# Kernel optimization log

Hardware: AMD Instinct MI355X
Metric: run time of the kernel (lower is better)

The kernel has to match this reference:

```python
import jax, jax.numpy as jnp
import numpy as np

NUM_ITER = 3
HEADS = 8
EPS = 1e-8

def _ln(x, g, b, eps=1e-5):
    mu = x.mean(-1, keepdims=True)
    var = ((x - mu) ** 2).mean(-1, keepdims=True)
    return (x - mu) * jax.lax.rsqrt(var + eps) * g + b

def setup_inputs() -> dict:
    key = jax.random.key(0)
    ks = jax.random.split(key, 10)
    B, Nkv, Din = 32, 4096, 256
    Nq, S, Hm = 16, 256, 512
    def xav(k, shape):
        lim = (6.0 / (shape[0] + shape[1])) ** 0.5
        return jax.random.uniform(k, shape, minval=-lim, maxval=lim, dtype=jnp.float32)
    return {
        "slots": jax.random.normal(ks[0], (Nq, S), dtype=jnp.float32),
        "inputs": jax.random.normal(ks[1], (B, Nkv, Din), dtype=jnp.float32),
        "norm_in_g": jnp.ones((Din,), jnp.float32), "norm_in_b": jnp.zeros((Din,), jnp.float32),
        "norm_slots_g": jnp.ones((S,), jnp.float32), "norm_slots_b": jnp.zeros((S,), jnp.float32),
        "norm_mlp_g": jnp.ones((S,), jnp.float32), "norm_mlp_b": jnp.zeros((S,), jnp.float32),
        "Wq": xav(ks[2], (S, S)), "Wk": xav(ks[3], (S, Din)), "Wv": xav(ks[4], (S, Din)),
        "gru_wih": xav(ks[5], (3 * S, S)),
        "gru_whh": jax.random.normal(ks[6], (3 * S, S), dtype=jnp.float32) * (1.0 / S ** 0.5),
        "gru_bih": jnp.zeros((3 * S,), jnp.float32), "gru_bhh": jnp.zeros((3 * S,), jnp.float32),
        "mlp_w1": xav(ks[7], (Hm, S)), "mlp_b1": jnp.zeros((Hm,), jnp.float32),
        "mlp_w2": xav(ks[8], (S, Hm)), "mlp_b2": jnp.zeros((S,), jnp.float32),
    }

def reference(slots, inputs, norm_in_g, norm_in_b, norm_slots_g, norm_slots_b,
              norm_mlp_g, norm_mlp_b, Wq, Wk, Wv, gru_wih, gru_whh, gru_bih, gru_bhh,
              mlp_w1, mlp_b1, mlp_w2, mlp_b2):
    B, Nkv, Din = inputs.shape
    Nq, S = slots.shape
    H = HEADS
    hd = S // H
    slots = jnp.broadcast_to(slots, (B, Nq, S))
    x = _ln(inputs, norm_in_g, norm_in_b)
    k = (x @ Wk.T).reshape(B, Nkv, H, hd).transpose(0, 2, 1, 3) * (hd ** -0.5)  # [B,H,Nkv,hd]
    v = (x @ Wv.T).reshape(B, Nkv, H, hd).transpose(0, 2, 1, 3)
    attn_vis = None
    for _ in range(NUM_ITER):
        slots_prev = slots
        s = _ln(slots, norm_slots_g, norm_slots_b)
        q = (s @ Wq.T).reshape(B, Nq, H, hd).transpose(0, 2, 1, 3)  # [B,H,Nq,hd]
        # logits [B,Nkv,H*Nq]; softmax jointly over heads and slots per key (slot-axis softmax)
        logits = jnp.einsum('bhkd,bhqd->bkhq', k, q).reshape(B, Nkv, H * Nq)
        attn = jax.nn.softmax(logits, axis=-1).reshape(B, Nkv, H, Nq).transpose(0, 2, 1, 3)  # [B,H,Nkv,Nq]
        attn_vis = attn.sum(1)  # [B,Nkv,Nq]
        attn_n = attn / (attn.sum(axis=2, keepdims=True) + EPS)  # normalize over keys
        updates = jnp.einsum('bhkq,bhkd->bqhd', attn_n, v).reshape(B, Nq, S)
        # GRUCell: gates order r,z,n
        xg = updates.reshape(-1, S)
        h = slots_prev.reshape(-1, S)
        gi = xg @ gru_wih.T + gru_bih
        gh = h @ gru_whh.T + gru_bhh
        ir, iz, inn = jnp.split(gi, 3, axis=-1)
        hr, hz, hn = jnp.split(gh, 3, axis=-1)
        r = jax.nn.sigmoid(ir + hr)
        z = jax.nn.sigmoid(iz + hz)
        n = jnp.tanh(inn + r * hn)
        slots = ((1.0 - z) * n + z * h).reshape(B, Nq, S)
        m = _ln(slots, norm_mlp_g, norm_mlp_b)
        slots = slots + (jax.nn.relu(m @ mlp_w1.T + mlp_b1) @ mlp_w2.T + mlp_b2)
    return (slots, attn_vis)
```

## Files before the change

kernel.cpp:

```cpp
#include <hip/hip_runtime.h>
#include <stdint.h>

typedef unsigned short u16;
typedef __attribute__((ext_vector_type(8))) _Float16 half8;
typedef __attribute__((ext_vector_type(4))) _Float16 half4;
typedef __attribute__((ext_vector_type(4))) float floatx4;

__device__ inline float bflo(unsigned u){ return __uint_as_float(u << 16); }
__device__ inline float bfhi(unsigned u){ return __uint_as_float(u & 0xffff0000u); }
__device__ inline float bf1(u16 v){ return __uint_as_float(((unsigned)v) << 16); }
__device__ inline u16 f2bf(float f){
  unsigned u = __float_as_uint(f);
  u += 0x7fffu + ((u >> 16) & 1u);
  return (u16)(u >> 16);
}
__device__ inline float dot8(uint4 w, float4 a, float4 b, float acc){
  acc = fmaf(bflo(w.x), a.x, acc); acc = fmaf(bfhi(w.x), a.y, acc);
  acc = fmaf(bflo(w.y), a.z, acc); acc = fmaf(bfhi(w.y), a.w, acc);
  acc = fmaf(bflo(w.z), b.x, acc); acc = fmaf(bfhi(w.z), b.y, acc);
  acc = fmaf(bflo(w.w), b.z, acc); acc = fmaf(bfhi(w.w), b.w, acc);
  return acc;
}

#define CW_SLOTS 0
#define CW_GIN   4096
#define CW_BIN   4352
#define CW_GS    4608
#define CW_BS    4864
#define CW_GM    5120
#define CW_BM    5376
#define CW_WQ    5632
#define CW_WK    71168
#define CW_WV    136704
#define CW_WIH   202240
#define CW_WHH   398848
#define CW_BIH   595456
#define CW_BHH   596224
#define CW_W1    596992
#define CW_B1    728064
#define CW_W2    728576
#define CW_B2    859648
#define CW_TOTAL 859904

__global__ void k_flag(const u16* __restrict__ probe, int* __restrict__ flag){
  int t = threadIdx.x;
  int bad = 0;
  #pragma unroll
  for (int i = 0; i < 4; i++){
    float x = bf1(probe[t + i * 256]);
    if (!(fabsf(x) < 1e6f)) bad = 1;
  }
  __shared__ int s;
  if (t == 0) s = 0;
  __syncthreads();
  if (bad) atomicOr(&s, 1);
  __syncthreads();
  if (t == 0) *flag = s;
}

struct CanonArgs { const void* p[18]; };

__global__ void k_canon(CanonArgs a, const int* __restrict__ flag, u16* __restrict__ cw){
  const int off[19] = {CW_SLOTS, CW_GIN, CW_BIN, CW_GS, CW_BS, CW_GM, CW_BM, CW_WQ,
                       CW_WK, CW_WV, CW_WIH, CW_WHH, CW_BIH, CW_BHH, CW_W1, CW_B1,
                       CW_W2, CW_B2, CW_TOTAL};
  int i = blockIdx.x * 256 + threadIdx.x;
  if (i >= CW_TOTAL) return;
  int f32m = *flag;
  int j = 0;
  while (i >= off[j + 1]) j++;
  int local = i - off[j];
  float v = f32m ? ((const float*)a.p[j])[local] : bf1(((const u16*)a.p[j])[local]);
  cw[i] = f2bf(v);
}

__global__ void k_init(const u16* __restrict__ cw, float* __restrict__ slots,
                       _Float16* __restrict__ wkvh)
{
  int idx = blockIdx.x * 256 + threadIdx.x;
  if (idx < 131072){
    float g = bf1(cw[CW_GIN + (idx & 255)]);
    wkvh[idx] = (_Float16)(bf1(cw[CW_WK + idx]) * g);
  } else {
    int i = idx - 131072;
    int d = i & 255;
    int q = (i >> 8) & 15;
    slots[i] = bf1(cw[CW_SLOTS + q * 256 + d]);
  }
}

__global__ void k_beta(const u16* __restrict__ cw, float* __restrict__ beta){
  int c = blockIdx.x * 256 + threadIdx.x;
  if (c >= 512) return;
  float a = 0.f;
  for (int d = 0; d < 256; d++)
    a = fmaf(bf1(cw[CW_BIN + d]), bf1(cw[CW_WK + c * 256 + d]), a);
  beta[c] = a;
}

__global__ void k_zero(float* __restrict__ p, int n){
  int i = blockIdx.x * 256 + threadIdx.x;
  if (i < n) p[i] = 0.f;
}

__global__ __launch_bounds__(256) void k0_stats(
    const void* __restrict__ inp, const int* __restrict__ flag, float2* __restrict__ stats)
{
  int f32m = *flag;
  int g = blockIdx.x * 256 + threadIdx.x;
  int row = g >> 4, l = g & 15;
  float sum = 0.f, sq = 0.f;
  if (f32m){
    const float* rp = (const float*)inp + row * 256 + l * 16;
    #pragma unroll
    for (int i = 0; i < 4; i++){
      float4 v = ((const float4*)rp)[i];
      sum += v.x + v.y + v.z + v.w;
      sq = fmaf(v.x, v.x, sq); sq = fmaf(v.y, v.y, sq);
      sq = fmaf(v.z, v.z, sq); sq = fmaf(v.w, v.w, sq);
    }
  } else {
    const u16* rp = (const u16*)inp + row * 256 + l * 16;
    #pragma unroll
    for (int i = 0; i < 2; i++){
      uint4 u = ((const uint4*)rp)[i];
      unsigned w[4] = {u.x, u.y, u.z, u.w};
      #pragma unroll
      for (int p = 0; p < 4; p++){
        float a = bflo(w[p]), b = bfhi(w[p]);
        sum += a + b; sq = fmaf(a, a, sq); sq = fmaf(b, b, sq);
      }
    }
  }
  #pragma unroll
  for (int m = 1; m < 16; m <<= 1){ sum += __shfl_xor(sum, m); sq += __shfl_xor(sq, m); }
  if (l == 0){
    float mu = sum * (1.f/256.f);
    float var = sq * (1.f/256.f) - mu * mu;
    stats[row] = make_float2(mu, rsqrtf(var + 1e-5f));
  }
}

__global__ __launch_bounds__(256) void k1_gemm(
    const void* __restrict__ inp, const int* __restrict__ flag,
    const float2* __restrict__ stats, const float* __restrict__ beta,
    const _Float16* __restrict__ wkvh, _Float16* __restrict__ kh, _Float16* __restrict__ vT)
{
  int f32m = *flag;
  int tid = threadIdx.x;
  int wv = tid >> 6, lane = tid & 63;
  int m16 = lane & 15, q4 = lane >> 4;
  int nb = blockIdx.y;
  long rowb0 = (long)blockIdx.x * 256;
  int colW = nb * 256 + wv * 64;

  half8 bf[4][8];
  #pragma unroll
  for (int nt = 0; nt < 4; nt++)
    #pragma unroll
    for (int s = 0; s < 8; s++)
      bf[nt][s] = *(const half8*)(wkvh + (colW + nt * 16 + m16) * 256 + s * 32 + q4 * 8);

  float bet[4];
  #pragma unroll
  for (int nt = 0; nt < 4; nt++) bet[nt] = beta[colW + nt * 16 + m16];

  for (int rt = 0; rt < 16; rt++){
    long rowb = rowb0 + rt * 16;
    long myRow = rowb + m16;
    float2 st = stats[myRow];
    float mu = st.x, rstd = st.y;

    half8 af[8];
    if (f32m){
      const float* rp = (const float*)inp + myRow * 256 + q4 * 8;
      #pragma unroll
      for (int s = 0; s < 8; s++){
        float4 x0 = *(const float4*)(rp + s * 32);
        float4 x1 = *(const float4*)(rp + s * 32 + 4);
        af[s][0] = (_Float16)((x0.x - mu) * rstd); af[s][1] = (_Float16)((x0.y - mu) * rstd);
        af[s][2] = (_Float16)((x0.z - mu) * rstd); af[s][3] = (_Float16)((x0.w - mu) * rstd);
        af[s][4] = (_Float16)((x1.x - mu) * rstd); af[s][5] = (_Float16)((x1.y - mu) * rstd);
        af[s][6] = (_Float16)((x1.z - mu) * rstd); af[s][7] = (_Float16)((x1.w - mu) * rstd);
      }
    } else {
      const u16* rp = (const u16*)inp + myRow * 256 + q4 * 8;
      #pragma unroll
      for (int s = 0; s < 8; s++){
        uint4 xu = *(const uint4*)(rp + s * 32);
        unsigned xw[4] = {xu.x, xu.y, xu.z, xu.w};
        #pragma unroll
        for (int p = 0; p < 4; p++){
          af[s][2*p]   = (_Float16)((bflo(xw[p]) - mu) * rstd);
          af[s][2*p+1] = (_Float16)((bfhi(xw[p]) - mu) * rstd);
        }
      }
    }

    floatx4 acc[4];
    #pragma unroll
    for (int nt = 0; nt < 4; nt++){
      acc[nt][0] = bet[nt]; acc[nt][1] = bet[nt]; acc[nt][2] = bet[nt]; acc[nt][3] = bet[nt];
    }
    #pragma unroll
    for (int s = 0; s < 8; s++)
      #pragma unroll
      for (int nt = 0; nt < 4; nt++)
        acc[nt] = __builtin_amdgcn_mfma_f32_16x16x32_f16(af[s], bf[nt][s], acc[nt], 0, 0, 0);

    if (nb == 0){
      long crow = rowb + q4 * 4;
      #pragma unroll
      for (int nt = 0; nt < 4; nt++)
        #pragma unroll
        for (int r = 0; r < 4; r++)
          kh[(crow + r) * 256 + colW + nt * 16 + m16] = (_Float16)acc[nt][r];
    } else {
      int b = (int)(rowb >> 12);
      int key = ((int)rowb & 4095) + q4 * 4;
      #pragma unroll
      for (int nt = 0; nt < 4; nt++){
        int cv = (colW - 256) + nt * 16 + m16;
        half4 pk;
        pk[0] = (_Float16)acc[nt][0]; pk[1] = (_Float16)acc[nt][1];
        pk[2] = (_Float16)acc[nt][2]; pk[3] = (_Float16)acc[nt][3];
        *(half4*)(vT + ((long)b * 256 + cv) * 4096 + key) = pk;
      }
    }
  }
}

__global__ __launch_bounds__(256) void k2_q(
    const float* __restrict__ slots, const u16* __restrict__ cw, _Float16* __restrict__ qh)
{
  const u16* gq = cw + CW_GS;
  const u16* bq = cw + CW_BS;
  const u16* Wq = cw + CW_WQ;
  int row = blockIdx.x, tid = threadIdx.x;
  int wv = tid >> 6, lane = tid & 63;
  float x = slots[row * 256 + tid];
  float s = x, s2 = x * x;
  #pragma unroll
  for (int m = 1; m < 64; m <<= 1){ s += __shfl_xor(s, m); s2 += __shfl_xor(s2, m); }
  __shared__ float red[8];
  if (lane == 0){ red[wv] = s; red[4 + wv] = s2; }
  __syncthreads();
  float tot  = red[0] + red[1] + red[2] + red[3];
  float tot2 = red[4] + red[5] + red[6] + red[7];
  float mu = tot * (1.f/256.f);
  float rstd = rsqrtf(tot2 * (1.f/256.f) - mu * mu + 1e-5f);
  __shared__ float sln[256];
  sln[tid] = (x - mu) * rstd * bf1(gq[tid]) + bf1(bq[tid]);
  __syncthreads();
  const u16* wr = Wq + tid * 256;
  float a = 0.f;
  for (int k = 0; k < 256; k += 8){
    uint4 wu = *(const uint4*)(wr + k);
    float4 l0 = *(const float4*)(sln + k);
    float4 l1 = *(const float4*)(sln + k + 4);
    a = dot8(wu, l0, l1, a);
  }
  qh[row * 256 + tid] = (_Float16)(a * 0.17677669529663687f);
}

__global__ __launch_bounds__(256) void k3_attn(
    const _Float16* __restrict__ kh, const _Float16* __restrict__ vT,
    const _Float16* __restrict__ qh,
    float* __restrict__ numer, float* __restrict__ denom,
    void* __restrict__ av_base, const int* __restrict__ flag, int lastIter)
{
  int f32m = *flag;
  int tid = threadIdx.x;
  int wv = tid >> 6, lane = tid & 63;
  int m16 = lane & 15, q4 = lane >> 4;
  int b = blockIdx.y, chunk = blockIdx.x;
  __shared__ float lds_l[32 * 129];

  half8 qf[2];
  #pragma unroll
  for (int hh = 0; hh < 2; hh++){
    int h = wv * 2 + hh;
    qf[hh] = *(const half8*)(qh + (b * 16 + m16) * 256 + h * 32 + q4 * 8);
  }
  float pd[2] = {0.f, 0.f};
  floatx4 un[2][2];
  #pragma unroll
  for (int hh = 0; hh < 2; hh++)
    #pragma unroll
    for (int dt = 0; dt < 2; dt++) un[hh][dt] = (floatx4)0.f;

  floatx4 z4 = (floatx4)0.f;
  for (int g4 = 0; g4 < 4; g4++){
    int key0 = chunk * 128 + g4 * 32;
    #pragma unroll
    for (int sub = 0; sub < 2; sub++){
      long rowb = (long)b * 4096 + key0 + sub * 16;
      #pragma unroll
      for (int hh = 0; hh < 2; hh++){
        int h = wv * 2 + hh;
        half8 af = *(const half8*)(kh + (rowb + m16) * 256 + h * 32 + q4 * 8);
        floatx4 d = __builtin_amdgcn_mfma_f32_16x16x32_f16(af, qf[hh], z4, 0, 0, 0);
        #pragma unroll
        for (int r = 0; r < 4; r++)
          lds_l[(sub * 16 + q4 * 4 + r) * 129 + h * 16 + m16] = d[r];
      }
    }
    __syncthreads();
    {
      int qq = tid & 15;
      #pragma unroll
      for (int half_ = 0; half_ < 2; half_++){
        int kk = (tid >> 4) + half_ * 16;
        float l[8];
        #pragma unroll
        for (int h8 = 0; h8 < 8; h8++) l[h8] = lds_l[kk * 129 + h8 * 16 + qq];
        float M = l[0];
        #pragma unroll
        for (int h8 = 1; h8 < 8; h8++) M = fmaxf(M, l[h8]);
        #pragma unroll
        for (int msk = 1; msk < 16; msk <<= 1) M = fmaxf(M, __shfl_xor(M, msk));
        float p[8], sl = 0.f;
        #pragma unroll
        for (int h8 = 0; h8 < 8; h8++){ p[h8] = __expf(l[h8] - M); sl += p[h8]; }
        float St = sl;
        #pragma unroll
        for (int msk = 1; msk < 16; msk <<= 1) St += __shfl_xor(St, msk);
        float rS = 1.f / St;
        #pragma unroll
        for (int h8 = 0; h8 < 8; h8++) lds_l[kk * 129 + h8 * 16 + qq] = p[h8] * rS;
        if (lastIter){
          long idx = 131072 + ((long)b * 4096 + key0 + kk) * 16 + qq;
          float av = sl * rS;
          if (f32m) ((float*)av_base)[idx] = av;
          else      ((u16*)av_base)[idx]   = f2bf(av);
        }
      }
    }
    __syncthreads();
    #pragma unroll
    for (int hh = 0; hh < 2; hh++){
      int h = wv * 2 + hh;
      float pv[8];
      #pragma unroll
      for (int j = 0; j < 8; j++) pv[j] = lds_l[(q4 * 8 + j) * 129 + h * 16 + m16];
      float ps = 0.f;
      #pragma unroll
      for (int j = 0; j < 8; j++) ps += pv[j];
      pd[hh] += ps;
      half8 bfr;
      #pragma unroll
      for (int j = 0; j < 8; j++) bfr[j] = (_Float16)pv[j];
      #pragma unroll
      for (int dt = 0; dt < 2; dt++){
        half8 afr = *(const half8*)(vT + ((long)b * 256 + h * 32 + dt * 16 + m16) * 4096 + key0 + q4 * 8);
        un[hh][dt] = __builtin_amdgcn_mfma_f32_16x16x32_f16(afr, bfr, un[hh][dt], 0, 0, 0);
      }
    }
    __syncthreads();
  }
  #pragma unroll
  for (int hh = 0; hh < 2; hh++){
    int h = wv * 2 + hh;
    float t = pd[hh];
    t += __shfl_xor(t, 16); t += __shfl_xor(t, 32);
    if (q4 == 0) atomicAdd(&denom[(b * 8 + h) * 16 + m16], t);
    #pragma unroll
    for (int dt = 0; dt < 2; dt++)
      #pragma unroll
      for (int r = 0; r < 4; r++)
        atomicAdd(&numer[((b * 8 + h) * 16 + m16) * 32 + dt * 16 + q4 * 4 + r], un[hh][dt][r]);
  }
}

__global__ __launch_bounds__(256) void k4a_gru(
    const float* __restrict__ slots, const float* __restrict__ numer, const float* __restrict__ denom,
    const u16* __restrict__ cw, float* __restrict__ mid)
{
  const u16* wih = cw + CW_WIH;
  const u16* whh = cw + CW_WHH;
  const u16* bih = cw + CW_BIH;
  const u16* bhh = cw + CW_BHH;
  int jc = blockIdx.x, rg = blockIdx.y;
  int tid = threadIdx.x;
  __shared__ float u_s[8][256];
  __shared__ float h_s[8][256];
  {
    int hh = tid >> 5, dh = tid & 31;
    for (int i = 0; i < 8; i++){
      int row = rg * 8 + i;
      int b = row >> 4, slot = row & 15;
      float den = denom[(b * 8 + hh) * 16 + slot] + 1e-8f;
      u_s[i][tid] = numer[((b * 8 + hh) * 16 + slot) * 32 + dh] / den;
      h_s[i][tid] = slots[row * 256 + tid];
    }
  }
  __syncthreads();
  int rl = tid >> 5, jl = tid & 31;
  int j = jc * 32 + jl;
  int row = rg * 8 + rl;
  const u16* wir = wih + j * 256;
  const u16* wiz = wih + (256 + j) * 256;
  const u16* win = wih + (512 + j) * 256;
  const u16* whr = whh + j * 256;
  const u16* whz = whh + (256 + j) * 256;
  const u16* whn = whh + (512 + j) * 256;
  float air = 0, aiz = 0, ain = 0, ahr = 0, ahz = 0, ahn = 0;
  for (int k = 0; k < 256; k += 8){
    float4 u0 = *(const float4*)(&u_s[rl][k]);
    float4 u1 = *(const float4*)(&u_s[rl][k + 4]);
    float4 h0 = *(const float4*)(&h_s[rl][k]);
    float4 h1 = *(const float4*)(&h_s[rl][k + 4]);
    air = dot8(*(const uint4*)(wir + k), u0, u1, air);
    aiz = dot8(*(const uint4*)(wiz + k), u0, u1, aiz);
    ain = dot8(*(const uint4*)(win + k), u0, u1, ain);
    ahr = dot8(*(const uint4*)(whr + k), h0, h1, ahr);
    ahz = dot8(*(const uint4*)(whz + k), h0, h1, ahz);
    ahn = dot8(*(const uint4*)(whn + k), h0, h1, ahn);
  }
  float gr = air + bf1(bih[j])       + ahr + bf1(bhh[j]);
  float gz = aiz + bf1(bih[256 + j]) + ahz + bf1(bhh[256 + j]);
  float r = 1.f / (1.f + __expf(-gr));
  float z = 1.f / (1.f + __expf(-gz));
  float nn = tanhf(ain + bf1(bih[512 + j]) + r * (ahn + bf1(bhh[512 + j])));
  float h = h_s[rl][j];
  mid[row * 256 + j] = (1.f - z) * nn + z * h;
}

__global__ __launch_bounds__(256) void k4b_mlp(
    const float* __restrict__ mid, const u16* __restrict__ cw,
    float* __restrict__ slots, void* __restrict__ out_base,
    const int* __restrict__ flag, int lastIter)
{
  int f32m = *flag;
  const u16* gm = cw + CW_GM;
  const u16* bm = cw + CW_BM;
  const u16* w1 = cw + CW_W1;
  const u16* b1 = cw + CW_B1;
  const u16* w2 = cw + CW_W2;
  const u16* b2 = cw + CW_B2;
  int row = blockIdx.x, tid = threadIdx.x;
  int wv = tid >> 6, lane = tid & 63;
  float x = mid[row * 256 + tid];
  float s = x, s2 = x * x;
  #pragma unroll
  for (int m = 1; m < 64; m <<= 1){ s += __shfl_xor(s, m); s2 += __shfl_xor(s2, m); }
  __shared__ float red[8];
  if (lane == 0){ red[wv] = s; red[4 + wv] = s2; }
  __syncthreads();
  float tot  = red[0] + red[1] + red[2] + red[3];
  float tot2 = red[4] + red[5] + red[6] + red[7];
  float mu = tot * (1.f/256.f);
  float rstd = rsqrtf(tot2 * (1.f/256.f) - mu * mu + 1e-5f);
  __shared__ float ls[256];
  __shared__ float h1[512];
  ls[tid] = (x - mu) * rstd * bf1(gm[tid]) + bf1(bm[tid]);
  __syncthreads();
  const u16* w1a = w1 + tid * 256;
  const u16* w1b = w1 + (tid + 256) * 256;
  float a0 = 0.f, a1 = 0.f;
  for (int k = 0; k < 256; k += 8){
    float4 l0 = *(const float4*)(ls + k);
    float4 l1 = *(const float4*)(ls + k + 4);
    a0 = dot8(*(const uint4*)(w1a + k), l0, l1, a0);
    a1 = dot8(*(const uint4*)(w1b + k), l0, l1, a1);
  }
  h1[tid]       = fmaxf(a0 + bf1(b1[tid]), 0.f);
  h1[tid + 256] = fmaxf(a1 + bf1(b1[tid + 256]), 0.f);
  __syncthreads();
  const u16* w2r = w2 + tid * 512;
  float a = 0.f;
  for (int k = 0; k < 512; k += 8){
    float4 l0 = *(const float4*)(h1 + k);
    float4 l1 = *(const float4*)(h1 + k + 4);
    a = dot8(*(const uint4*)(w2r + k), l0, l1, a);
  }
  float res = x + a + bf1(b2[tid]);
  slots[row * 256 + tid] = res;
  if (lastIter){
    int idx = row * 256 + tid;
    if (f32m) ((float*)out_base)[idx] = res;
    else      ((u16*)out_base)[idx]   = f2bf(res);
  }
}

extern "C" void kernel_launch(void* const* d_in, const int* in_sizes, int n_in,
                              void* d_out, int out_size, void* d_ws, size_t ws_size,
                              hipStream_t stream)
{
  char* ws = (char*)d_ws;
  int*  flagp    = (int*)ws;
  u16*  cw       = (u16*)(ws + 256);
  _Float16* qh   = (_Float16*)(ws + 1720064);
  _Float16* wkvh = (_Float16*)(ws + 1982208);
  float* slots   = (float*)(ws + 2244352);
  float* mid     = (float*)(ws + 2768640);
  float* numer   = (float*)(ws + 3292928);
  float* denom   = (float*)(ws + 3817216);
  _Float16* kh   = (_Float16*)(ws + 3833600);
  _Float16* vT   = (_Float16*)(ws + 70942464);
  float2* stats  = (float2*)(ws + 2768640);
  float*  beta   = (float*)(ws + 3817216);

  CanonArgs ca;
  ca.p[0]  = d_in[0];   ca.p[1]  = d_in[2];   ca.p[2]  = d_in[3];
  ca.p[3]  = d_in[4];   ca.p[4]  = d_in[5];   ca.p[5]  = d_in[6];
  ca.p[6]  = d_in[7];   ca.p[7]  = d_in[8];   ca.p[8]  = d_in[9];
  ca.p[9]  = d_in[10];  ca.p[10] = d_in[11];  ca.p[11] = d_in[12];
  ca.p[12] = d_in[13];  ca.p[13] = d_in[14];  ca.p[14] = d_in[15];
  ca.p[15] = d_in[16];  ca.p[16] = d_in[17];  ca.p[17] = d_in[18];

  k_flag<<<1, 256, 0, stream>>>((const u16*)d_in[1], flagp);
  k_canon<<<(CW_TOTAL + 255) / 256, 256, 0, stream>>>(ca, flagp, cw);
  k_init<<<1024, 256, 0, stream>>>(cw, slots, wkvh);
  k_beta<<<2, 256, 0, stream>>>(cw, beta);
  k0_stats<<<8192, 256, 0, stream>>>(d_in[1], flagp, stats);
  k1_gemm<<<dim3(512, 2), 256, 0, stream>>>(d_in[1], flagp, stats, beta, wkvh, kh, vT);
  for (int it = 0; it < 3; it++){
    int last = (it == 2) ? 1 : 0;
    k2_q<<<512, 256, 0, stream>>>(slots, cw, qh);
    k_zero<<<528, 256, 0, stream>>>(numer, 135168);
    k3_attn<<<dim3(32, 32), 256, 0, stream>>>(kh, vT, qh, numer, denom, d_out, flagp, last);
    k4a_gru<<<dim3(8, 64), 256, 0, stream>>>(slots, numer, denom, cw, mid);
    k4b_mlp<<<512, 256, 0, stream>>>(mid, cw, slots, d_out, flagp, last);
  }
}
```

Measured before the change: 928.5 us.

## Fuse LayerNorm stats into K/V GEMM and replace attention atomics with partial-sum reduction

```diff
diff --git a/kernel.cpp b/kernel.cpp
--- a/kernel.cpp
+++ b/kernel.cpp
@@ -42,6 +42,9 @@
 #define CW_B2    859648
 #define CW_TOTAL 859904
 
+#define NPART 16
+#define PART_STRIDE 135168
+
 __global__ void k_flag(const u16* __restrict__ probe, int* __restrict__ flag){
   int t = threadIdx.x;
   int bad = 0;
@@ -103,47 +106,9 @@
   if (i < n) p[i] = 0.f;
 }
 
-__global__ __launch_bounds__(256) void k0_stats(
-    const void* __restrict__ inp, const int* __restrict__ flag, float2* __restrict__ stats)
-{
-  int f32m = *flag;
-  int g = blockIdx.x * 256 + threadIdx.x;
-  int row = g >> 4, l = g & 15;
-  float sum = 0.f, sq = 0.f;
-  if (f32m){
-    const float* rp = (const float*)inp + row * 256 + l * 16;
-    #pragma unroll
-    for (int i = 0; i < 4; i++){
-      float4 v = ((const float4*)rp)[i];
-      sum += v.x + v.y + v.z + v.w;
-      sq = fmaf(v.x, v.x, sq); sq = fmaf(v.y, v.y, sq);
-      sq = fmaf(v.z, v.z, sq); sq = fmaf(v.w, v.w, sq);
-    }
-  } else {
-    const u16* rp = (const u16*)inp + row * 256 + l * 16;
-    #pragma unroll
-    for (int i = 0; i < 2; i++){
-      uint4 u = ((const uint4*)rp)[i];
-      unsigned w[4] = {u.x, u.y, u.z, u.w};
-      #pragma unroll
-      for (int p = 0; p < 4; p++){
-        float a = bflo(w[p]), b = bfhi(w[p]);
-        sum += a + b; sq = fmaf(a, a, sq); sq = fmaf(b, b, sq);
-      }
-    }
-  }
-  #pragma unroll
-  for (int m = 1; m < 16; m <<= 1){ sum += __shfl_xor(sum, m); sq += __shfl_xor(sq, m); }
-  if (l == 0){
-    float mu = sum * (1.f/256.f);
-    float var = sq * (1.f/256.f) - mu * mu;
-    stats[row] = make_float2(mu, rsqrtf(var + 1e-5f));
-  }
-}
-
 __global__ __launch_bounds__(256) void k1_gemm(
     const void* __restrict__ inp, const int* __restrict__ flag,
-    const float2* __restrict__ stats, const float* __restrict__ beta,
+    const float* __restrict__ beta,
     const _Float16* __restrict__ wkvh, _Float16* __restrict__ kh, _Float16* __restrict__ vT)
 {
   int f32m = *flag;
@@ -154,21 +119,54 @@
   long rowb0 = (long)blockIdx.x * 256;
   int colW = nb * 256 + wv * 64;
 
-  half8 bf[4][8];
+  __shared__ float2 sst[256];
+
+  {
+    float sum = 0.f, sq = 0.f;
+    if (f32m){
+      const float* rp = (const float*)inp + (rowb0 + tid) * 256;
+      #pragma unroll 4
+      for (int i = 0; i < 64; i++){
+        float4 v = ((const float4*)rp)[i];
+        sum += v.x + v.y + v.z + v.w;
+        sq = fmaf(v.x, v.x, sq); sq = fmaf(v.y, v.y, sq);
+        sq = fmaf(v.z, v.z, sq); sq = fmaf(v.w, v.w, sq);
+      }
+    } else {
+      const u16* rp = (const u16*)inp + (rowb0 + tid) * 256;
+      #pragma unroll 4
+      for (int i = 0; i < 32; i++){
+        uint4 u = ((const uint4*)rp)[i];
+        unsigned w[4] = {u.x, u.y, u.z, u.w};
+        #pragma unroll
+        for (int p = 0; p < 4; p++){
+          float a = bflo(w[p]), b = bfhi(w[p]);
+          sum += a + b; sq = fmaf(a, a, sq); sq = fmaf(b, b, sq);
+        }
+      }
+    }
+    float mu = sum * (1.f/256.f);
+    float var = sq * (1.f/256.f) - mu * mu;
+    sst[tid] = make_float2(mu, rsqrtf(var + 1e-5f));
+  }
+
+  half8 bfr[4][8];
   #pragma unroll
   for (int nt = 0; nt < 4; nt++)
     #pragma unroll
     for (int s = 0; s < 8; s++)
-      bf[nt][s] = *(const half8*)(wkvh + (colW + nt * 16 + m16) * 256 + s * 32 + q4 * 8);
+      bfr[nt][s] = *(const half8*)(wkvh + (colW + nt * 16 + m16) * 256 + s * 32 + q4 * 8);
 
   float bet[4];
   #pragma unroll
   for (int nt = 0; nt < 4; nt++) bet[nt] = beta[colW + nt * 16 + m16];
+
+  __syncthreads();
 
   for (int rt = 0; rt < 16; rt++){
     long rowb = rowb0 + rt * 16;
     long myRow = rowb + m16;
-    float2 st = stats[myRow];
+    float2 st = sst[rt * 16 + m16];
     float mu = st.x, rstd = st.y;
 
     half8 af[8];
@@ -206,7 +204,7 @@
     for (int s = 0; s < 8; s++)
       #pragma unroll
       for (int nt = 0; nt < 4; nt++)
-        acc[nt] = __builtin_amdgcn_mfma_f32_16x16x32_f16(af[s], bf[nt][s], acc[nt], 0, 0, 0);
+        acc[nt] = __builtin_amdgcn_mfma_f32_16x16x32_f16(af[s], bfr[nt][s], acc[nt], 0, 0, 0);
 
     if (nb == 0){
       long crow = rowb + q4 * 4;
@@ -267,6 +265,7 @@
     const _Float16* __restrict__ kh, const _Float16* __restrict__ vT,
     const _Float16* __restrict__ qh,
     float* __restrict__ numer, float* __restrict__ denom,
+    float* __restrict__ part, int use_part,
     void* __restrict__ av_base, const int* __restrict__ flag, int lastIter)
 {
   int f32m = *flag;
@@ -290,8 +289,8 @@
     for (int dt = 0; dt < 2; dt++) un[hh][dt] = (floatx4)0.f;
 
   floatx4 z4 = (floatx4)0.f;
-  for (int g4 = 0; g4 < 4; g4++){
-    int key0 = chunk * 128 + g4 * 32;
+  for (int g4 = 0; g4 < 8; g4++){
+    int key0 = chunk * 256 + g4 * 32;
     #pragma unroll
     for (int sub = 0; sub < 2; sub++){
       long rowb = (long)b * 4096 + key0 + sub * 16;
@@ -358,18 +357,41 @@
     }
     __syncthreads();
   }
-  #pragma unroll
-  for (int hh = 0; hh < 2; hh++){
-    int h = wv * 2 + hh;
-    float t = pd[hh];
-    t += __shfl_xor(t, 16); t += __shfl_xor(t, 32);
-    if (q4 == 0) atomicAdd(&denom[(b * 8 + h) * 16 + m16], t);
-    #pragma unroll
-    for (int dt = 0; dt < 2; dt++)
-      #pragma unroll
-      for (int r = 0; r < 4; r++)
-        atomicAdd(&numer[((b * 8 + h) * 16 + m16) * 32 + dt * 16 + q4 * 4 + r], un[hh][dt][r]);
-  }
+  if (use_part){
+    float* pn = part + (long)chunk * PART_STRIDE;
+    #pragma unroll
+    for (int hh = 0; hh < 2; hh++){
+      int h = wv * 2 + hh;
+      float t = pd[hh];
+      t += __shfl_xor(t, 16); t += __shfl_xor(t, 32);
+      if (q4 == 0) pn[131072 + (b * 8 + h) * 16 + m16] = t;
+      #pragma unroll
+      for (int dt = 0; dt < 2; dt++)
+        *(floatx4*)(&pn[((b * 8 + h) * 16 + m16) * 32 + dt * 16 + q4 * 4]) = un[hh][dt];
+    }
+  } else {
+    #pragma unroll
+    for (int hh = 0; hh < 2; hh++){
+      int h = wv * 2 + hh;
+      float t = pd[hh];
+      t += __shfl_xor(t, 16); t += __shfl_xor(t, 32);
+      if (q4 == 0) atomicAdd(&denom[(b * 8 + h) * 16 + m16], t);
+      #pragma unroll
+      for (int dt = 0; dt < 2; dt++)
+        #pragma unroll
+        for (int r = 0; r < 4; r++)
+          atomicAdd(&numer[((b * 8 + h) * 16 + m16) * 32 + dt * 16 + q4 * 4 + r], un[hh][dt][r]);
+    }
+  }
+}
+
+__global__ void k_reduce(const float* __restrict__ part, float* __restrict__ numer){
+  int i = blockIdx.x * 256 + threadIdx.x;
+  if (i >= PART_STRIDE) return;
+  float s = 0.f;
+  #pragma unroll
+  for (int c = 0; c < NPART; c++) s += part[(long)c * PART_STRIDE + i];
+  numer[i] = s;
 }
 
 __global__ __launch_bounds__(256) void k4a_gru(
@@ -498,8 +520,10 @@
   float* denom   = (float*)(ws + 3817216);
   _Float16* kh   = (_Float16*)(ws + 3833600);
   _Float16* vT   = (_Float16*)(ws + 70942464);
-  float2* stats  = (float2*)(ws + 2768640);
-  float*  beta   = (float*)(ws + 3817216);
+  float* part    = (float*)(ws + 138051328);
+  float* beta    = (float*)(ws + 3817216);
+
+  int use_part = (ws_size >= 146702080UL) ? 1 : 0;
 
   CanonArgs ca;
   ca.p[0]  = d_in[0];   ca.p[1]  = d_in[2];   ca.p[2]  = d_in[3];
@@ -513,13 +537,14 @@
   k_canon<<<(CW_TOTAL + 255) / 256, 256, 0, stream>>>(ca, flagp, cw);
   k_init<<<1024, 256, 0, stream>>>(cw, slots, wkvh);
   k_beta<<<2, 256, 0, stream>>>(cw, beta);
-  k0_stats<<<8192, 256, 0, stream>>>(d_in[1], flagp, stats);
-  k1_gemm<<<dim3(512, 2), 256, 0, stream>>>(d_in[1], flagp, stats, beta, wkvh, kh, vT);
+  k1_gemm<<<dim3(512, 2), 256, 0, stream>>>(d_in[1], flagp, beta, wkvh, kh, vT);
   for (int it = 0; it < 3; it++){
     int last = (it == 2) ? 1 : 0;
     k2_q<<<512, 256, 0, stream>>>(slots, cw, qh);
-    k_zero<<<528, 256, 0, stream>>>(numer, 135168);
-    k3_attn<<<dim3(32, 32), 256, 0, stream>>>(kh, vT, qh, numer, denom, d_out, flagp, last);
+    if (!use_part) k_zero<<<528, 256, 0, stream>>>(numer, 135168);
+    k3_attn<<<dim3(16, 32), 256, 0, stream>>>(kh, vT, qh, numer, denom, part, use_part,
+                                              d_out, flagp, last);
+    if (use_part) k_reduce<<<528, 256, 0, stream>>>(part, numer);
     k4a_gru<<<dim3(8, 64), 256, 0, stream>>>(slots, numer, denom, cw, mid);
     k4b_mlp<<<512, 256, 0, stream>>>(mid, cw, slots, d_out, flagp, last);
   }
```

Result: faster. 821.7 us (-11.5%).

## Replace attention atomics with per-chunk partial buffers and a reduction kernel

Applied to the files above, without the earlier changes.

```diff
diff --git a/kernel.cpp b/kernel.cpp
--- a/kernel.cpp
+++ b/kernel.cpp
@@ -42,6 +42,8 @@
 #define CW_B2    859648
 #define CW_TOTAL 859904
 
+#define PART_STRIDE 135168
+
 __global__ void k_flag(const u16* __restrict__ probe, int* __restrict__ flag){
   int t = threadIdx.x;
   int bad = 0;
@@ -151,21 +153,21 @@
   int wv = tid >> 6, lane = tid & 63;
   int m16 = lane & 15, q4 = lane >> 4;
   int nb = blockIdx.y;
-  long rowb0 = (long)blockIdx.x * 256;
+  long rowb0 = (long)blockIdx.x * 128;
   int colW = nb * 256 + wv * 64;
 
-  half8 bf[4][8];
+  half8 bfr[4][8];
   #pragma unroll
   for (int nt = 0; nt < 4; nt++)
     #pragma unroll
     for (int s = 0; s < 8; s++)
-      bf[nt][s] = *(const half8*)(wkvh + (colW + nt * 16 + m16) * 256 + s * 32 + q4 * 8);
+      bfr[nt][s] = *(const half8*)(wkvh + (colW + nt * 16 + m16) * 256 + s * 32 + q4 * 8);
 
   float bet[4];
   #pragma unroll
   for (int nt = 0; nt < 4; nt++) bet[nt] = beta[colW + nt * 16 + m16];
 
-  for (int rt = 0; rt < 16; rt++){
+  for (int rt = 0; rt < 8; rt++){
     long rowb = rowb0 + rt * 16;
     long myRow = rowb + m16;
     float2 st = stats[myRow];
@@ -206,7 +208,7 @@
     for (int s = 0; s < 8; s++)
       #pragma unroll
       for (int nt = 0; nt < 4; nt++)
-        acc[nt] = __builtin_amdgcn_mfma_f32_16x16x32_f16(af[s], bf[nt][s], acc[nt], 0, 0, 0);
+        acc[nt] = __builtin_amdgcn_mfma_f32_16x16x32_f16(af[s], bfr[nt][s], acc[nt], 0, 0, 0);
 
     if (nb == 0){
       long crow = rowb + q4 * 4;
@@ -267,6 +269,7 @@
     const _Float16* __restrict__ kh, const _Float16* __restrict__ vT,
     const _Float16* __restrict__ qh,
     float* __restrict__ numer, float* __restrict__ denom,
+    float* __restrict__ part, int use_part, int g4count,
     void* __restrict__ av_base, const int* __restrict__ flag, int lastIter)
 {
   int f32m = *flag;
@@ -274,6 +277,7 @@
   int wv = tid >> 6, lane = tid & 63;
   int m16 = lane & 15, q4 = lane >> 4;
   int b = blockIdx.y, chunk = blockIdx.x;
+  int kpc = g4count * 32;
   __shared__ float lds_l[32 * 129];
 
   half8 qf[2];
@@ -290,8 +294,8 @@
     for (int dt = 0; dt < 2; dt++) un[hh][dt] = (floatx4)0.f;
 
   floatx4 z4 = (floatx4)0.f;
-  for (int g4 = 0; g4 < 4; g4++){
-    int key0 = chunk * 128 + g4 * 32;
+  for (int g4 = 0; g4 < g4count; g4++){
+    int key0 = chunk * kpc + g4 * 32;
     #pragma unroll
     for (int sub = 0; sub < 2; sub++){
       long rowb = (long)b * 4096 + key0 + sub * 16;
@@ -358,18 +362,40 @@
     }
     __syncthreads();
   }
-  #pragma unroll
-  for (int hh = 0; hh < 2; hh++){
-    int h = wv * 2 + hh;
-    float t = pd[hh];
-    t += __shfl_xor(t, 16); t += __shfl_xor(t, 32);
-    if (q4 == 0) atomicAdd(&denom[(b * 8 + h) * 16 + m16], t);
-    #pragma unroll
-    for (int dt = 0; dt < 2; dt++)
-      #pragma unroll
-      for (int r = 0; r < 4; r++)
-        atomicAdd(&numer[((b * 8 + h) * 16 + m16) * 32 + dt * 16 + q4 * 4 + r], un[hh][dt][r]);
-  }
+  if (use_part){
+    float* pn = part + (long)chunk * PART_STRIDE;
+    #pragma unroll
+    for (int hh = 0; hh < 2; hh++){
+      int h = wv * 2 + hh;
+      float t = pd[hh];
+      t += __shfl_xor(t, 16); t += __shfl_xor(t, 32);
+      if (q4 == 0) pn[131072 + (b * 8 + h) * 16 + m16] = t;
+      #pragma unroll
+      for (int dt = 0; dt < 2; dt++)
+        *(floatx4*)(&pn[((b * 8 + h) * 16 + m16) * 32 + dt * 16 + q4 * 4]) = un[hh][dt];
+    }
+  } else {
+    #pragma unroll
+    for (int hh = 0; hh < 2; hh++){
+      int h = wv * 2 + hh;
+      float t = pd[hh];
+      t += __shfl_xor(t, 16); t += __shfl_xor(t, 32);
+      if (q4 == 0) atomicAdd(&denom[(b * 8 + h) * 16 + m16], t);
+      #pragma unroll
+      for (int dt = 0; dt < 2; dt++)
+        #pragma unroll
+        for (int r = 0; r < 4; r++)
+          atomicAdd(&numer[((b * 8 + h) * 16 + m16) * 32 + dt * 16 + q4 * 4 + r], un[hh][dt][r]);
+    }
+  }
+}
+
+__global__ void k_reduce(const float* __restrict__ part, float* __restrict__ numer, int npart){
+  int i = blockIdx.x * 256 + threadIdx.x;
+  if (i >= PART_STRIDE) return;
+  float s = 0.f;
+  for (int c = 0; c < npart; c++) s += part[(long)c * PART_STRIDE + i];
+  numer[i] = s;
 }
 
 __global__ __launch_bounds__(256) void k4a_gru(
@@ -498,8 +524,19 @@
   float* denom   = (float*)(ws + 3817216);
   _Float16* kh   = (_Float16*)(ws + 3833600);
   _Float16* vT   = (_Float16*)(ws + 70942464);
+  float* part    = (float*)(ws + 138051328);
   float2* stats  = (float2*)(ws + 2768640);
   float*  beta   = (float*)(ws + 3817216);
+
+  const size_t base_end = 138051328UL;
+  const size_t per_chunk = (size_t)PART_STRIDE * 4;
+  int npart = 0;
+  if      (ws_size >= base_end + 16 * per_chunk) npart = 16;
+  else if (ws_size >= base_end +  8 * per_chunk) npart = 8;
+  else if (ws_size >= base_end +  4 * per_chunk) npart = 4;
+  int use_part = (npart > 0);
+  int nchunks = use_part ? npart : 16;
+  int g4count = (4096 / nchunks) / 32;
 
   CanonArgs ca;
   ca.p[0]  = d_in[0];   ca.p[1]  = d_in[2];   ca.p[2]  = d_in[3];
@@ -514,12 +551,14 @@
   k_init<<<1024, 256, 0, stream>>>(cw, slots, wkvh);
   k_beta<<<2, 256, 0, stream>>>(cw, beta);
   k0_stats<<<8192, 256, 0, stream>>>(d_in[1], flagp, stats);
-  k1_gemm<<<dim3(512, 2), 256, 0, stream>>>(d_in[1], flagp, stats, beta, wkvh, kh, vT);
+  k1_gemm<<<dim3(1024, 2), 256, 0, stream>>>(d_in[1], flagp, stats, beta, wkvh, kh, vT);
   for (int it = 0; it < 3; it++){
     int last = (it == 2) ? 1 : 0;
     k2_q<<<512, 256, 0, stream>>>(slots, cw, qh);
-    k_zero<<<528, 256, 0, stream>>>(numer, 135168);
-    k3_attn<<<dim3(32, 32), 256, 0, stream>>>(kh, vT, qh, numer, denom, d_out, flagp, last);
+    if (!use_part) k_zero<<<528, 256, 0, stream>>>(numer, 135168);
+    k3_attn<<<dim3(nchunks, 32), 256, 0, stream>>>(kh, vT, qh, numer, denom, part,
+                                                   use_part, g4count, d_out, flagp, last);
+    if (use_part) k_reduce<<<528, 256, 0, stream>>>(part, numer, npart);
     k4a_gru<<<dim3(8, 64), 256, 0, stream>>>(slots, numer, denom, cw, mid);
     k4b_mlp<<<512, 256, 0, stream>>>(mid, cw, slots, d_out, flagp, last);
   }
```

After: 812.1 us. -12.5%, faster.

## Replace attention numerator atomics with per-chunk partials and separate reduce

Applied to the files above, without the earlier changes.

```diff
diff --git a/kernel.cpp b/kernel.cpp
--- a/kernel.cpp
+++ b/kernel.cpp
@@ -151,21 +151,21 @@
   int wv = tid >> 6, lane = tid & 63;
   int m16 = lane & 15, q4 = lane >> 4;
   int nb = blockIdx.y;
-  long rowb0 = (long)blockIdx.x * 256;
+  long rowb0 = (long)blockIdx.x * 128;
   int colW = nb * 256 + wv * 64;
 
-  half8 bf[4][8];
+  half8 bfr[4][8];
   #pragma unroll
   for (int nt = 0; nt < 4; nt++)
     #pragma unroll
     for (int s = 0; s < 8; s++)
-      bf[nt][s] = *(const half8*)(wkvh + (colW + nt * 16 + m16) * 256 + s * 32 + q4 * 8);
+      bfr[nt][s] = *(const half8*)(wkvh + (colW + nt * 16 + m16) * 256 + s * 32 + q4 * 8);
 
   float bet[4];
   #pragma unroll
   for (int nt = 0; nt < 4; nt++) bet[nt] = beta[colW + nt * 16 + m16];
 
-  for (int rt = 0; rt < 16; rt++){
+  for (int rt = 0; rt < 8; rt++){
     long rowb = rowb0 + rt * 16;
     long myRow = rowb + m16;
     float2 st = stats[myRow];
@@ -206,7 +206,7 @@
     for (int s = 0; s < 8; s++)
       #pragma unroll
       for (int nt = 0; nt < 4; nt++)
-        acc[nt] = __builtin_amdgcn_mfma_f32_16x16x32_f16(af[s], bf[nt][s], acc[nt], 0, 0, 0);
+        acc[nt] = __builtin_amdgcn_mfma_f32_16x16x32_f16(af[s], bfr[nt][s], acc[nt], 0, 0, 0);
 
     if (nb == 0){
       long crow = rowb + q4 * 4;
@@ -266,8 +266,8 @@
 __global__ __launch_bounds__(256) void k3_attn(
     const _Float16* __restrict__ kh, const _Float16* __restrict__ vT,
     const _Float16* __restrict__ qh,
-    float* __restrict__ numer, float* __restrict__ denom,
-    void* __restrict__ av_base, const int* __restrict__ flag, int lastIter)
+    float* __restrict__ denom, void* __restrict__ out_scratch,
+    const int* __restrict__ flag)
 {
   int f32m = *flag;
   int tid = threadIdx.x;
@@ -290,8 +290,8 @@
     for (int dt = 0; dt < 2; dt++) un[hh][dt] = (floatx4)0.f;
 
   floatx4 z4 = (floatx4)0.f;
-  for (int g4 = 0; g4 < 4; g4++){
-    int key0 = chunk * 128 + g4 * 32;
+  for (int g4 = 0; g4 < 8; g4++){
+    int key0 = chunk * 256 + g4 * 32;
     #pragma unroll
     for (int sub = 0; sub < 2; sub++){
       long rowb = (long)b * 4096 + key0 + sub * 16;
@@ -328,12 +328,6 @@
         float rS = 1.f / St;
         #pragma unroll
         for (int h8 = 0; h8 < 8; h8++) lds_l[kk * 129 + h8 * 16 + qq] = p[h8] * rS;
-        if (lastIter){
-          long idx = 131072 + ((long)b * 4096 + key0 + kk) * 16 + qq;
-          float av = sl * rS;
-          if (f32m) ((float*)av_base)[idx] = av;
-          else      ((u16*)av_base)[idx]   = f2bf(av);
-        }
       }
     }
     __syncthreads();
@@ -358,6 +352,8 @@
     }
     __syncthreads();
   }
+  _Float16* pp = (_Float16*)((u16*)out_scratch + (f32m ? 262144 : 131072))
+                 + (long)chunk * 131072;
   #pragma unroll
   for (int hh = 0; hh < 2; hh++){
     int h = wv * 2 + hh;
@@ -365,10 +361,86 @@
     t += __shfl_xor(t, 16); t += __shfl_xor(t, 32);
     if (q4 == 0) atomicAdd(&denom[(b * 8 + h) * 16 + m16], t);
     #pragma unroll
-    for (int dt = 0; dt < 2; dt++)
-      #pragma unroll
-      for (int r = 0; r < 4; r++)
-        atomicAdd(&numer[((b * 8 + h) * 16 + m16) * 32 + dt * 16 + q4 * 4 + r], un[hh][dt][r]);
+    for (int dt = 0; dt < 2; dt++){
+      half4 st;
+      #pragma unroll
+      for (int r = 0; r < 4; r++) st[r] = (_Float16)un[hh][dt][r];
+      *(half4*)(pp + ((b * 8 + h) * 16 + m16) * 32 + dt * 16 + q4 * 4) = st;
+    }
+  }
+}
+
+__global__ void k_reduce(const void* __restrict__ out_scratch, const int* __restrict__ flag,
+                         float* __restrict__ numer){
+  int i = blockIdx.x * 256 + threadIdx.x;
+  int f32m = *flag;
+  const _Float16* pp = (const _Float16*)((const u16*)out_scratch + (f32m ? 262144 : 131072));
+  float s = 0.f;
+  #pragma unroll
+  for (int c = 0; c < 16; c++) s += (float)pp[(long)c * 131072 + i];
+  numer[i] = s;
+}
+
+__global__ __launch_bounds__(256) void k3_av(
+    const _Float16* __restrict__ kh, const _Float16* __restrict__ qh,
+    void* __restrict__ av_base, const int* __restrict__ flag)
+{
+  int f32m = *flag;
+  int tid = threadIdx.x;
+  int wv = tid >> 6, lane = tid & 63;
+  int m16 = lane & 15, q4 = lane >> 4;
+  int b = blockIdx.y, chunk = blockIdx.x;
+  __shared__ float lds_l[32 * 129];
+
+  half8 qf[2];
+  #pragma unroll
+  for (int hh = 0; hh < 2; hh++){
+    int h = wv * 2 + hh;
+    qf[hh] = *(const half8*)(qh + (b * 16 + m16) * 256 + h * 32 + q4 * 8);
+  }
+  floatx4 z4 = (floatx4)0.f;
+  for (int g4 = 0; g4 < 8; g4++){
+    int key0 = chunk * 256 + g4 * 32;
+    #pragma unroll
+    for (int sub = 0; sub < 2; sub++){
+      long rowb = (long)b * 4096 + key0 + sub * 16;
+      #pragma unroll
+      for (int hh = 0; hh < 2; hh++){
+        int h = wv * 2 + hh;
+        half8 af = *(const half8*)(kh + (rowb + m16) * 256 + h * 32 + q4 * 8);
+        floatx4 d = __builtin_amdgcn_mfma_f32_16x16x32_f16(af, qf[hh], z4, 0, 0, 0);
+        #pragma unroll
+        for (int r = 0; r < 4; r++)
+          lds_l[(sub * 16 + q4 * 4 + r) * 129 + h * 16 + m16] = d[r];
+      }
+    }
+    __syncthreads();
+    {
+      int qq = tid & 15;
+      #pragma unroll
+      for (int half_ = 0; half_ < 2; half_++){
+        int kk = (tid >> 4) + half_ * 16;
+        float l[8];
+        #pragma unroll
+        for (int h8 = 0; h8 < 8; h8++) l[h8] = lds_l[kk * 129 + h8 * 16 + qq];
+        float M = l[0];
+        #pragma unroll
+        for (int h8 = 1; h8 < 8; h8++) M = fmaxf(M, l[h8]);
+        #pragma unroll
+        for (int msk = 1; msk < 16; msk <<= 1) M = fmaxf(M, __shfl_xor(M, msk));
+        float sl = 0.f;
+        #pragma unroll
+        for (int h8 = 0; h8 < 8; h8++) sl += __expf(l[h8] - M);
+        float St = sl;
+        #pragma unroll
+        for (int msk = 1; msk < 16; msk <<= 1) St += __shfl_xor(St, msk);
+        float av = sl / St;
+        long idx = 131072 + ((long)b * 4096 + key0 + kk) * 16 + qq;
+        if (f32m) ((float*)av_base)[idx] = av;
+        else      ((u16*)av_base)[idx]   = f2bf(av);
+      }
+    }
+    __syncthreads();
   }
 }
 
@@ -514,12 +586,14 @@
   k_init<<<1024, 256, 0, stream>>>(cw, slots, wkvh);
   k_beta<<<2, 256, 0, stream>>>(cw, beta);
   k0_stats<<<8192, 256, 0, stream>>>(d_in[1], flagp, stats);
-  k1_gemm<<<dim3(512, 2), 256, 0, stream>>>(d_in[1], flagp, stats, beta, wkvh, kh, vT);
+  k1_gemm<<<dim3(1024, 2), 256, 0, stream>>>(d_in[1], flagp, stats, beta, wkvh, kh, vT);
   for (int it = 0; it < 3; it++){
     int last = (it == 2) ? 1 : 0;
     k2_q<<<512, 256, 0, stream>>>(slots, cw, qh);
-    k_zero<<<528, 256, 0, stream>>>(numer, 135168);
-    k3_attn<<<dim3(32, 32), 256, 0, stream>>>(kh, vT, qh, numer, denom, d_out, flagp, last);
+    k_zero<<<16, 256, 0, stream>>>(denom, 4096);
+    k3_attn<<<dim3(16, 32), 256, 0, stream>>>(kh, vT, qh, denom, d_out, flagp);
+    k_reduce<<<512, 256, 0, stream>>>(d_out, flagp, numer);
+    if (last) k3_av<<<dim3(16, 32), 256, 0, stream>>>(kh, qh, d_out, flagp);
     k4a_gru<<<dim3(8, 64), 256, 0, stream>>>(slots, numer, denom, cw, mid);
     k4b_mlp<<<512, 256, 0, stream>>>(mid, cw, slots, d_out, flagp, last);
   }
```

Result: faster. 811.2 us (-12.6%).
